# Performance work log

Measured on AMD Instinct MI355X. Metric: run time of the kernel, lower is better.

## Reference

```python
import jax, jax.numpy as jnp
import numpy as np

B, S, D, H = 4, 2048, 1024, 16
HD = D // H
EPS = 1e-5

def _ln(x, g, b):
    mu = jnp.mean(x, axis=-1, keepdims=True)
    var = jnp.mean(jnp.square(x - mu), axis=-1, keepdims=True)
    return (x - mu) * jax.lax.rsqrt(var + EPS) * g + b

def setup_inputs() -> dict:
    key = jax.random.key(0)
    ks = jax.random.split(key, 6)
    W = 0.02  # GPT-2 style init scale keeps softmax unsaturated
    causal = jnp.tril(jnp.ones((S, S), dtype=bool))
    mask = jnp.where(causal, 0.0, -1e9).astype(jnp.float32)[None, None]
    return {
        "x": jax.random.normal(ks[0], (B, S, D), jnp.float32),
        "attention_mask": mask,
        "ln1_g": jnp.ones((D,), jnp.float32),
        "ln1_b": jnp.zeros((D,), jnp.float32),
        "w_qkv": jax.random.normal(ks[1], (D, 3 * D), jnp.float32) * W,
        "b_qkv": jnp.zeros((3 * D,), jnp.float32),
        "w_ao": jax.random.normal(ks[2], (D, D), jnp.float32) * W,
        "b_ao": jnp.zeros((D,), jnp.float32),
        "ln2_g": jnp.ones((D,), jnp.float32),
        "ln2_b": jnp.zeros((D,), jnp.float32),
        "w_fc": jax.random.normal(ks[3], (D, 4 * D), jnp.float32) * W,
        "b_fc": jnp.zeros((4 * D,), jnp.float32),
        "w_out": jax.random.normal(ks[4], (4 * D, D), jnp.float32) * W,
        "b_out": jnp.zeros((D,), jnp.float32),
    }

def reference(x, attention_mask, ln1_g, ln1_b, w_qkv, b_qkv, w_ao, b_ao,
              ln2_g, ln2_b, w_fc, b_fc, w_out, b_out):
    b, s, d = x.shape
    h = _ln(x, ln1_g, ln1_b)
    qkv = h @ w_qkv + b_qkv  # [B,S,3D]
    q, k, v = jnp.split(qkv, 3, axis=-1)
    def heads(t):  # [B,S,D] -> [B,H,S,HD]
        return t.reshape(b, s, H, HD).transpose(0, 2, 1, 3)
    q, k, v = heads(q), heads(k), heads(v)
    att = jnp.einsum('bhqd,bhkd->bhqk', q, k) / jnp.sqrt(jnp.float32(HD))
    att = att + attention_mask
    att = jax.nn.softmax(att, axis=-1)
    out = jnp.einsum('bhqk,bhkd->bhqd', att, v)
    out = out.transpose(0, 2, 1, 3).reshape(b, s, d)
    x = x + out @ w_ao + b_ao
    h2 = _ln(x, ln2_g, ln2_b)
    # torch nn.GELU() default is exact erf gelu
    mlp = jax.nn.gelu(h2 @ w_fc + b_fc, approximate=False) @ w_out + b_out
    return x + mlp
```

## Files before the change

kernel.cpp:

```cpp
#include <hip/hip_runtime.h>

typedef unsigned short u16;
typedef __attribute__((ext_vector_type(8))) short short8;
typedef __attribute__((ext_vector_type(4))) float floatx4;
typedef __attribute__((ext_vector_type(4))) unsigned short ushort4_t;

#define S_LEN 2048
#define DMODEL 1024
#define NHEAD 16
#define HDIM 64

__device__ __forceinline__ u16 f2bf(float f) {
    union { float f; unsigned u; } v; v.f = f;
    unsigned u = v.u;
    unsigned r = (u + 0x7fffu + ((u >> 16) & 1u)) >> 16;
    return (u16)r;
}

__device__ __forceinline__ u16 f2bf_fast(float f) {
    union { float f; unsigned u; } v; v.f = f;
    return (u16)((v.u + 0x8000u) >> 16);
}

__device__ __forceinline__ void gld_lds16(const u16* g, u16* l) {
    __builtin_amdgcn_global_load_lds((const __attribute__((address_space(1))) void*)g,
                                     (__attribute__((address_space(3))) void*)l,
                                     16, 0, 0);
}

__global__ __launch_bounds__(256) void ln_kernel(
    const float* __restrict__ x, const float* __restrict__ g,
    const float* __restrict__ b, u16* __restrict__ out)
{
    int row = blockIdx.x;
    int tid = threadIdx.x;
    const float4* xr = (const float4*)(x + (size_t)row * DMODEL);
    float4 v = xr[tid];
    float s  = v.x + v.y + v.z + v.w;
    float s2 = v.x * v.x + v.y * v.y + v.z * v.z + v.w * v.w;
    #pragma unroll
    for (int off = 1; off < 64; off <<= 1) {
        s  += __shfl_xor(s, off, 64);
        s2 += __shfl_xor(s2, off, 64);
    }
    __shared__ float red[2][4];
    int w = tid >> 6, lane = tid & 63;
    if (lane == 0) { red[0][w] = s; red[1][w] = s2; }
    __syncthreads();
    s  = red[0][0] + red[0][1] + red[0][2] + red[0][3];
    s2 = red[1][0] + red[1][1] + red[1][2] + red[1][3];
    float mu  = s * (1.0f / DMODEL);
    float var = s2 * (1.0f / DMODEL) - mu * mu;
    float inv = rsqrtf(var + 1e-5f);
    const float4* gr = (const float4*)g;
    const float4* br = (const float4*)b;
    float4 gv = gr[tid], bv = br[tid];
    u16* o = out + (size_t)row * DMODEL + tid * 4;
    o[0] = f2bf((v.x - mu) * inv * gv.x + bv.x);
    o[1] = f2bf((v.y - mu) * inv * gv.y + bv.y);
    o[2] = f2bf((v.z - mu) * inv * gv.z + bv.z);
    o[3] = f2bf((v.w - mu) * inv * gv.w + bv.w);
}

__global__ __launch_bounds__(256) void transpose_cast(
    const float* __restrict__ w, u16* __restrict__ wt, int K, int N)
{
    __shared__ float t[32][33];
    int n0 = blockIdx.x * 32, k0 = blockIdx.y * 32;
    int x = threadIdx.x, y = threadIdx.y;
    #pragma unroll
    for (int j = y; j < 32; j += 8)
        t[j][x] = w[(size_t)(k0 + j) * N + n0 + x];
    __syncthreads();
    #pragma unroll
    for (int j = y; j < 32; j += 8)
        wt[(size_t)(n0 + j) * K + k0 + x] = f2bf(t[x][j]);
}

template<int MODE>
__global__ __launch_bounds__(256) void gemm_bt(
    const u16* __restrict__ A, const u16* __restrict__ BT,
    int M, int N, int K,
    const float* __restrict__ bias, const float* __restrict__ res,
    float* __restrict__ fout,
    u16* __restrict__ o0, u16* __restrict__ o1, u16* __restrict__ o2)
{
    __shared__ __attribute__((aligned(16))) u16 As[2][128 * 64];
    __shared__ __attribute__((aligned(16))) u16 Bs[2][128 * 64];
    int tid = threadIdx.x;
    int lane = tid & 63, w = tid >> 6;
    int wm = (w >> 1) * 64, wn = (w & 1) * 64;
    int l15 = lane & 15, quad = lane >> 4;
    int rowBase = blockIdx.y * 128, colBase = blockIdx.x * 128;

    floatx4 acc[4][4] = {};

    const u16* pa[4];
    const u16* pbt[4];
    int scb[4];
    #pragma unroll
    for (int i = 0; i < 4; ++i) {
        int c  = i * 256 + tid;
        int r  = c >> 3;
        int cs = ((c & 7) ^ (r & 7)) * 8;
        pa[i]  = A  + (size_t)(rowBase + r) * K + cs;
        pbt[i] = BT + (size_t)(colBase + r) * K + cs;
        scb[i] = (i * 256 + (tid & 0xC0)) * 8;
    }

    int KT = K >> 6;

    #pragma unroll
    for (int i = 0; i < 4; ++i) {
        gld_lds16(pa[i],  &As[0][0] + scb[i]);
        gld_lds16(pbt[i], &Bs[0][0] + scb[i]);
    }

    for (int kt = 0; kt < KT; ++kt) {
        __syncthreads();

        if (kt + 1 < KT) {
            u16* abuf = &As[(kt + 1) & 1][0];
            u16* bbuf = &Bs[(kt + 1) & 1][0];
            #pragma unroll
            for (int i = 0; i < 4; ++i) {
                pa[i]  += 64;
                pbt[i] += 64;
                gld_lds16(pa[i],  abuf + scb[i]);
                gld_lds16(pbt[i], bbuf + scb[i]);
            }
        }

        const u16* as = &As[kt & 1][0];
        const u16* bs = &Bs[kt & 1][0];
        #pragma unroll
        for (int ks = 0; ks < 2; ++ks) {
            int sw = (((ks * 4 + quad) ^ (l15 & 7))) * 8;
            short8 af[4], bf[4];
            #pragma unroll
            for (int im = 0; im < 4; ++im)
                af[im] = *(const short8*)(as + (wm + im * 16 + l15) * 64 + sw);
            #pragma unroll
            for (int in = 0; in < 4; ++in)
                bf[in] = *(const short8*)(bs + (wn + in * 16 + l15) * 64 + sw);
            #pragma unroll
            for (int im = 0; im < 4; ++im)
                #pragma unroll
                for (int in = 0; in < 4; ++in)
                    acc[im][in] = __builtin_amdgcn_mfma_f32_16x16x32_bf16(af[im], bf[in], acc[im][in], 0, 0, 0);
        }
    }

    if (MODE == 0) {
        int t = colBase >> 10;
        int cb1023 = colBase & 1023;
        if (t == 2) {
            #pragma unroll
            for (int im = 0; im < 4; ++im) {
                int gr0 = rowBase + wm + im * 16 + quad * 4;
                int bb2 = gr0 >> 11, ss = gr0 & 2047;
                #pragma unroll
                for (int in = 0; in < 4; ++in) {
                    int gc = colBase + wn + in * 16 + l15;
                    int rr = cb1023 + wn + in * 16 + l15;
                    int hh = rr >> 6, hd = rr & 63;
                    float bv = bias[gc];
                    ushort4_t pk;
                    pk.x = f2bf_fast(acc[im][in][0] + bv);
                    pk.y = f2bf_fast(acc[im][in][1] + bv);
                    pk.z = f2bf_fast(acc[im][in][2] + bv);
                    pk.w = f2bf_fast(acc[im][in][3] + bv);
                    *(ushort4_t*)(o1 + ((size_t)(bb2 * NHEAD + hh) * HDIM + hd) * S_LEN + ss) = pk;
                }
            }
        } else {
            u16* qb = o0 + (size_t)t * 8388608;
            float sc = (t == 0) ? 0.125f : 1.0f;
            #pragma unroll
            for (int im = 0; im < 4; ++im) {
                #pragma unroll
                for (int in = 0; in < 4; ++in) {
                    #pragma unroll
                    for (int r = 0; r < 4; ++r) {
                        int gr = rowBase + wm + im * 16 + quad * 4 + r;
                        int gc = colBase + wn + in * 16 + l15;
                        float v = (acc[im][in][r] + bias[gc]) * sc;
                        int rr = cb1023 + wn + in * 16 + l15;
                        int hh = rr >> 6, hd = rr & 63;
                        int bb2 = gr >> 11, ss = gr & 2047;
                        qb[(((size_t)(bb2 * NHEAD + hh) * S_LEN + ss) * HDIM) + hd] = f2bf_fast(v);
                    }
                }
            }
        }
    } else {
        #pragma unroll
        for (int im = 0; im < 4; ++im) {
            #pragma unroll
            for (int in = 0; in < 4; ++in) {
                #pragma unroll
                for (int r = 0; r < 4; ++r) {
                    int gr = rowBase + wm + im * 16 + quad * 4 + r;
                    int gc = colBase + wn + in * 16 + l15;
                    float v = acc[im][in][r] + bias[gc];
                    if (MODE == 2) {
                        float p = v * (1.59576912f + 0.07135481f * v * v);
                        float e = __expf(-p);
                        float gl = v * __builtin_amdgcn_rcpf(1.0f + e);
                        o0[(size_t)gr * N + gc] = f2bf_fast(gl);
                    } else {
                        fout[(size_t)gr * N + gc] = v + res[(size_t)gr * N + gc];
                    }
                }
            }
        }
    }
}

__global__ __launch_bounds__(256) void flash_attn(
    const u16* __restrict__ Q, const u16* __restrict__ Kb,
    const u16* __restrict__ Vt, u16* __restrict__ O)
{
    __shared__ __attribute__((aligned(16))) u16 Ks[2][64 * 64];
    __shared__ __attribute__((aligned(16))) u16 Vs[2][64 * 64];
    __shared__ __attribute__((aligned(16))) u16 Pl[4][2][16][64];
    int tid = threadIdx.x;
    int lane = tid & 63, w = tid >> 6;
    int l15 = lane & 15, quad = lane >> 4;
    int bh = blockIdx.x;
    int pp = blockIdx.y;
    int bb = bh >> 4, h = bh & 15;

    const u16* Kp0 = Kb + (size_t)bh * S_LEN * HDIM;
    const u16* Vp  = Vt + (size_t)bh * HDIM * S_LEN;

    int rstage = lane >> 3;
    int cstage = ((lane & 7) ^ rstage) * 8;
    int vrow0  = w * 8 + rstage;

    int ms[2] = {pp, 15 - pp};
    int pb = 0;

    #pragma unroll
    for (int i = 0; i < 2; ++i) {
        int row = i * 32 + vrow0;
        gld_lds16(Kp0 + row * HDIM + cstage, &Ks[0][0] + i * 2048 + w * 512);
        gld_lds16(Vp + (size_t)row * S_LEN + cstage, &Vs[0][0] + i * 2048 + w * 512);
    }

    #pragma unroll 1
    for (int sel = 0; sel < 2; ++sel) {
        int m = ms[sel];
        int q0 = m * 128;

        const u16* Qp = Q + ((size_t)bh * S_LEN + q0 + w * 16) * HDIM;
        short8 aq0[2], aq1[2];
        #pragma unroll
        for (int ks = 0; ks < 2; ++ks) {
            aq0[ks] = *(const short8*)(Qp + l15 * HDIM + ks * 32 + quad * 8);
            aq1[ks] = *(const short8*)(Qp + 64 * HDIM + l15 * HDIM + ks * 32 + quad * 8);
        }

        floatx4 acc_o0[4] = {}, acc_o1[4] = {};
        float rs0[4] = {0.f, 0.f, 0.f, 0.f};
        float rs1[4] = {0.f, 0.f, 0.f, 0.f};

        int KT = 2 * m + 2;

        auto softmax_store = [&](floatx4 (&sa)[4], float (&rs)[4], int st, bool diag) {
            #pragma unroll
            for (int nt = 0; nt < 4; ++nt) {
                int wc = nt * 16 + l15;
                int wchunk = wc >> 3, woff = wc & 7;
                #pragma unroll
                for (int r = 0; r < 4; ++r) {
                    float sv = sa[nt][r];
                    if (diag) {
                        int qr = w * 16 + quad * 4 + r;
                        if (wc > qr) sv = -1e30f;
                    }
                    float pv = __expf(sv);
                    rs[r] += pv;
                    int row = quad * 4 + r;
                    Pl[w][st][row][((wchunk ^ (row & 7)) << 3) + woff] = f2bf_fast(pv);
                }
            }
        };

        #pragma unroll 1
        for (int kt = 0; kt < KT; ++kt) {
            __syncthreads();
            int cur = pb;

            int nk = (kt + 1 < KT) ? (kt + 1) : ((sel < 1) ? 0 : -1);
            if (nk >= 0) {
                pb ^= 1;
                const u16* Kg = Kp0 + (size_t)nk * 64 * HDIM;
                const u16* Vg = Vp + nk * 64;
                u16* kb_ = &Ks[pb][0];
                u16* vb_ = &Vs[pb][0];
                #pragma unroll
                for (int i = 0; i < 2; ++i) {
                    int row = i * 32 + vrow0;
                    gld_lds16(Kg + row * HDIM + cstage, kb_ + i * 2048 + w * 512);
                    gld_lds16(Vg + (size_t)row * S_LEN + cstage, vb_ + i * 2048 + w * 512);
                }
            }

            const u16* kcur = &Ks[cur][0];
            const u16* vcur = &Vs[cur][0];

            bool a0 = (kt < KT - 1);

            floatx4 s0a[4] = {}, s1a[4] = {};
            __builtin_amdgcn_s_setprio(1);
            #pragma unroll
            for (int nt = 0; nt < 4; ++nt) {
                #pragma unroll
                for (int ks = 0; ks < 2; ++ks) {
                    int sw = ((ks * 4 + quad) ^ (l15 & 7)) * 8;
                    short8 bk = *(const short8*)(kcur + (nt * 16 + l15) * 64 + sw);
                    s0a[nt] = __builtin_amdgcn_mfma_f32_16x16x32_bf16(aq0[ks], bk, s0a[nt], 0, 0, 0);
                    s1a[nt] = __builtin_amdgcn_mfma_f32_16x16x32_bf16(aq1[ks], bk, s1a[nt], 0, 0, 0);
                }
            }
            __builtin_amdgcn_s_setprio(0);

            if (a0) softmax_store(s0a, rs0, 0, kt == KT - 2);
            softmax_store(s1a, rs1, 1, kt == KT - 1);

            short8 pf0[2] = {}, pf1[2];
            if (a0) {
                #pragma unroll
                for (int ks = 0; ks < 2; ++ks) {
                    int pc = ((ks * 4 + quad) ^ (l15 & 7)) * 8;
                    pf0[ks] = *(const short8*)(&Pl[w][0][l15][pc]);
                }
            }
            #pragma unroll
            for (int ks = 0; ks < 2; ++ks) {
                int pc = ((ks * 4 + quad) ^ (l15 & 7)) * 8;
                pf1[ks] = *(const short8*)(&Pl[w][1][l15][pc]);
            }

            __builtin_amdgcn_s_setprio(1);
            #pragma unroll
            for (int nt = 0; nt < 4; ++nt) {
                #pragma unroll
                for (int ks = 0; ks < 2; ++ks) {
                    int sw = ((ks * 4 + quad) ^ (l15 & 7)) * 8;
                    short8 bv = *(const short8*)(vcur + (nt * 16 + l15) * 64 + sw);
                    acc_o0[nt] = __builtin_amdgcn_mfma_f32_16x16x32_bf16(pf0[ks], bv, acc_o0[nt], 0, 0, 0);
                    acc_o1[nt] = __builtin_amdgcn_mfma_f32_16x16x32_bf16(pf1[ks], bv, acc_o1[nt], 0, 0, 0);
                }
            }
            __builtin_amdgcn_s_setprio(0);
        }

        float inv0[4], inv1[4];
        #pragma unroll
        for (int r = 0; r < 4; ++r) {
            float sm0 = rs0[r], sm1 = rs1[r];
            #pragma unroll
            for (int off = 1; off < 16; off <<= 1) {
                sm0 += __shfl_xor(sm0, off, 64);
                sm1 += __shfl_xor(sm1, off, 64);
            }
            inv0[r] = 1.0f / sm0;
            inv1[r] = 1.0f / sm1;
        }

        #pragma unroll
        for (int nt = 0; nt < 4; ++nt) {
            #pragma unroll
            for (int r = 0; r < 4; ++r) {
                int qr = q0 + w * 16 + quad * 4 + r;
                int hd = nt * 16 + l15;
                O[((size_t)bb * S_LEN + qr) * DMODEL + h * HDIM + hd] = f2bf(acc_o0[nt][r] * inv0[r]);
                O[((size_t)bb * S_LEN + qr + 64) * DMODEL + h * HDIM + hd] = f2bf(acc_o1[nt][r] * inv1[r]);
            }
        }
    }
}

extern "C" void kernel_launch(void* const* d_in, const int* in_sizes, int n_in,
                              void* d_out, int out_size, void* d_ws, size_t ws_size,
                              hipStream_t stream)
{
    const float* x    = (const float*)d_in[0];
    const float* ln1g = (const float*)d_in[2];
    const float* ln1b = (const float*)d_in[3];
    const float* wqkv = (const float*)d_in[4];
    const float* bqkv = (const float*)d_in[5];
    const float* wao  = (const float*)d_in[6];
    const float* bao  = (const float*)d_in[7];
    const float* ln2g = (const float*)d_in[8];
    const float* ln2b = (const float*)d_in[9];
    const float* wfc  = (const float*)d_in[10];
    const float* bfc  = (const float*)d_in[11];
    const float* wout = (const float*)d_in[12];
    const float* bout = (const float*)d_in[13];
    float* out = (float*)d_out;

    char* ws = (char*)d_ws;
    u16* wqkvT = (u16*)(ws + 0);
    u16* waoT  = (u16*)(ws + 6291456);
    u16* wfcT  = (u16*)(ws + 8388608);
    u16* woutT = (u16*)(ws + 16777216);
    u16* hb    = (u16*)(ws + 25165824);
    u16* QKVb  = (u16*)(ws + 41943040);
    u16* Vtb   = (u16*)(ws + 92274688);
    u16* Gb    = (u16*)(ws + 41943040);

    u16* Qb   = QKVb;
    u16* Kbuf = QKVb + 8388608;

    transpose_cast<<<dim3(3072/32, 1024/32), dim3(32, 8), 0, stream>>>(wqkv, wqkvT, 1024, 3072);
    transpose_cast<<<dim3(1024/32, 1024/32), dim3(32, 8), 0, stream>>>(wao,  waoT,  1024, 1024);
    transpose_cast<<<dim3(4096/32, 1024/32), dim3(32, 8), 0, stream>>>(wfc,  wfcT,  1024, 4096);
    transpose_cast<<<dim3(1024/32, 4096/32), dim3(32, 8), 0, stream>>>(wout, woutT, 4096, 1024);

    ln_kernel<<<8192, 256, 0, stream>>>(x, ln1g, ln1b, hb);

    gemm_bt<0><<<dim3(3072/128, 8192/128), 256, 0, stream>>>(
        hb, wqkvT, 8192, 3072, 1024, bqkv, nullptr, nullptr, QKVb, Vtb, nullptr);

    flash_attn<<<dim3(64, 8), 256, 0, stream>>>(Qb, Kbuf, Vtb, hb);

    gemm_bt<1><<<dim3(1024/128, 8192/128), 256, 0, stream>>>(
        hb, waoT, 8192, 1024, 1024, bao, x, out, nullptr, nullptr, nullptr);

    ln_kernel<<<8192, 256, 0, stream>>>(out, ln2g, ln2b, hb);

    gemm_bt<2><<<dim3(4096/128, 8192/128), 256, 0, stream>>>(
        hb, wfcT, 8192, 4096, 1024, bfc, nullptr, nullptr, Gb, nullptr, nullptr);

    gemm_bt<3><<<dim3(1024/128, 8192/128), 256, 0, stream>>>(
        Gb, woutT, 8192, 1024, 4096, bout, out, out, nullptr, nullptr, nullptr);
}
```

Baseline: 498.0 us.

## Add 256x256 8-wave ping-pong GEMM for QKV and FC projections

Adds a new 512-thread GEMM kernel with 256x256 output tiles, double-buffered LDS split into halves, and an eight-phase schedule that interleaves global-to-LDS prefetch with MFMA quadrants, using barriers and s_setprio. The QKV and FC1+GELU GEMMs now use it, while the older 128x128 kernel is reduced to the residual-add epilogue for the remaining GEMMs. The larger tiles are meant to raise arithmetic intensity and overlap memory with compute. In exchange, register pressure and LDS use are higher, and fewer blocks are launched for the QKV shape.

Result: slower. 511.0 us (+2.6%).

```diff
diff --git a/kernel.cpp b/kernel.cpp
--- a/kernel.cpp
+++ b/kernel.cpp
@@ -151,25 +151,152 @@
         }
     }
 
+    #pragma unroll
+    for (int im = 0; im < 4; ++im) {
+        #pragma unroll
+        for (int in = 0; in < 4; ++in) {
+            #pragma unroll
+            for (int r = 0; r < 4; ++r) {
+                int gr = rowBase + wm + im * 16 + quad * 4 + r;
+                int gc = colBase + wn + in * 16 + l15;
+                float v = acc[im][in][r] + bias[gc];
+                fout[(size_t)gr * N + gc] = v + res[(size_t)gr * N + gc];
+            }
+        }
+    }
+}
+
+template<int MODE>
+__global__ __launch_bounds__(512, 2) void gemm256(
+    const u16* __restrict__ A, const u16* __restrict__ BT,
+    int M, int N, int K,
+    const float* __restrict__ bias,
+    u16* __restrict__ o0, u16* __restrict__ o1)
+{
+    __shared__ __attribute__((aligned(16))) u16 As[2][2][128 * 64];
+    __shared__ __attribute__((aligned(16))) u16 Bs[2][2][128 * 64];
+    int tid = threadIdx.x;
+    int lane = tid & 63, w = tid >> 6;
+    int wrow = w >> 2, wcol = w & 3;
+    int l15 = lane & 15, quad = lane >> 4;
+    int rowBase = blockIdx.y * 256, colBase = blockIdx.x * 256;
+    int nrb = (wcol & 1) * 64;
+
+    int swz[2] = { (quad ^ (l15 & 7)) * 8, ((4 + quad) ^ (l15 & 7)) * 8 };
+
+    int cid0 = tid, cid1 = 512 + tid;
+    int r0 = cid0 >> 3, r1 = cid1 >> 3;
+    unsigned cs0 = (unsigned)(((cid0 & 7) ^ (r0 & 7)) * 8);
+    unsigned cs1 = (unsigned)(((cid1 & 7) ^ (r1 & 7)) * 8);
+    unsigned aoff0 = (unsigned)((rowBase + r0) * K) + cs0;
+    unsigned aoff1 = (unsigned)((rowBase + r1) * K) + cs1;
+    unsigned boff0 = (unsigned)((colBase + r0) * K) + cs0;
+    unsigned boff1 = (unsigned)((colBase + r1) * K) + cs1;
+    unsigned ldo0 = (unsigned)(cid0 * 8), ldo1 = (unsigned)(cid1 * 8);
+    unsigned hK = (unsigned)(128 * K);
+
+    floatx4 acc[8][4] = {};
+    short8 af[4][2], bfL[2][2], bfH[2][2];
+
+    int KT = K >> 6;
+
+#define STG_A(db, tt, h) do { unsigned tb_ = (unsigned)(tt) * 64u + (h) * hK;      \
+    gld_lds16(A + aoff0 + tb_, &As[db][h][0] + ldo0);                              \
+    gld_lds16(A + aoff1 + tb_, &As[db][h][0] + ldo1); } while (0)
+#define STG_B(db, tt, h) do { unsigned tb_ = (unsigned)(tt) * 64u + (h) * hK;      \
+    gld_lds16(BT + boff0 + tb_, &Bs[db][h][0] + ldo0);                             \
+    gld_lds16(BT + boff1 + tb_, &Bs[db][h][0] + ldo1); } while (0)
+#define LDS_A(buf, MFB) do { const u16* ap_ = &As[buf][wrow][0];                   \
+    _Pragma("unroll") for (int m_ = 0; m_ < 4; ++m_) {                             \
+      af[m_][0] = *(const short8*)(ap_ + (((MFB) + m_) * 16 + l15) * 64 + swz[0]); \
+      af[m_][1] = *(const short8*)(ap_ + (((MFB) + m_) * 16 + l15) * 64 + swz[1]); } } while (0)
+#define LDS_B(buf, NFP, dst) do { const u16* bp_ = &Bs[buf][wcol >> 1][0];         \
+    _Pragma("unroll") for (int n_ = 0; n_ < 2; ++n_) {                             \
+      dst[n_][0] = *(const short8*)(bp_ + (nrb + ((NFP) * 2 + n_) * 16 + l15) * 64 + swz[0]); \
+      dst[n_][1] = *(const short8*)(bp_ + (nrb + ((NFP) * 2 + n_) * 16 + l15) * 64 + swz[1]); } } while (0)
+#define MFMA_Q(MFB, NFP, bsrc) do { __builtin_amdgcn_s_setprio(1);                 \
+    _Pragma("unroll") for (int m_ = 0; m_ < 4; ++m_)                               \
+    _Pragma("unroll") for (int n_ = 0; n_ < 2; ++n_) {                             \
+      acc[(MFB) + m_][(NFP) * 2 + n_] = __builtin_amdgcn_mfma_f32_16x16x32_bf16(af[m_][0], bsrc[n_][0], acc[(MFB) + m_][(NFP) * 2 + n_], 0, 0, 0); \
+      acc[(MFB) + m_][(NFP) * 2 + n_] = __builtin_amdgcn_mfma_f32_16x16x32_bf16(af[m_][1], bsrc[n_][1], acc[(MFB) + m_][(NFP) * 2 + n_], 0, 0, 0); } \
+    __builtin_amdgcn_s_setprio(0); } while (0)
+#define PH_MID() do { __builtin_amdgcn_s_barrier();                                \
+    asm volatile("s_waitcnt lgkmcnt(0)" ::: "memory"); } while (0)
+#define PH_END() __builtin_amdgcn_s_barrier()
+
+    STG_A(0, 0, 0); STG_A(0, 0, 1);
+    STG_B(0, 0, 0); STG_B(0, 0, 1);
+    STG_B(1, 1, 0); STG_B(1, 1, 1);
+    asm volatile("s_waitcnt vmcnt(4)" ::: "memory");
+    __builtin_amdgcn_s_barrier();
+
+    for (int t = 0; t < KT; t += 2) {
+        int t2 = (t + 2 < KT) ? t + 2 : KT - 1;
+        int t3 = (t + 3 < KT) ? t + 3 : KT - 1;
+
+        LDS_A(0, 0); LDS_B(0, 0, bfL);
+        STG_A(1, t + 1, 0);
+        PH_MID(); MFMA_Q(0, 0, bfL); PH_END();
+
+        LDS_B(0, 1, bfH);
+        STG_A(1, t + 1, 1);
+        PH_MID(); MFMA_Q(0, 1, bfH); PH_END();
+
+        LDS_A(0, 4);
+        STG_B(0, t2, 0);
+        PH_MID(); MFMA_Q(4, 1, bfH); PH_END();
+
+        STG_B(0, t2, 1);
+        asm volatile("s_waitcnt vmcnt(4)" ::: "memory");
+        PH_MID(); MFMA_Q(4, 0, bfL); PH_END();
+
+        LDS_A(1, 0); LDS_B(1, 0, bfL);
+        STG_A(0, t2, 0);
+        PH_MID(); MFMA_Q(0, 0, bfL); PH_END();
+
+        LDS_B(1, 1, bfH);
+        STG_A(0, t2, 1);
+        PH_MID(); MFMA_Q(0, 1, bfH); PH_END();
+
+        LDS_A(1, 4);
+        STG_B(1, t3, 0);
+        PH_MID(); MFMA_Q(4, 1, bfH); PH_END();
+
+        STG_B(1, t3, 1);
+        asm volatile("s_waitcnt vmcnt(4)" ::: "memory");
+        PH_MID(); MFMA_Q(4, 0, bfL); PH_END();
+    }
+    asm volatile("s_waitcnt vmcnt(0)" ::: "memory");
+
+#undef STG_A
+#undef STG_B
+#undef LDS_A
+#undef LDS_B
+#undef MFMA_Q
+#undef PH_MID
+#undef PH_END
+
+    int wr0 = rowBase + wrow * 128 + quad * 4;
+    int wc0 = colBase + wcol * 64 + l15;
     if (MODE == 0) {
         int t = colBase >> 10;
-        int cb1023 = colBase & 1023;
+        int cb1023 = (colBase & 1023) + wcol * 64;
         if (t == 2) {
             #pragma unroll
-            for (int im = 0; im < 4; ++im) {
-                int gr0 = rowBase + wm + im * 16 + quad * 4;
+            for (int mf = 0; mf < 8; ++mf) {
+                int gr0 = wr0 + mf * 16;
                 int bb2 = gr0 >> 11, ss = gr0 & 2047;
                 #pragma unroll
-                for (int in = 0; in < 4; ++in) {
-                    int gc = colBase + wn + in * 16 + l15;
-                    int rr = cb1023 + wn + in * 16 + l15;
+                for (int nf = 0; nf < 4; ++nf) {
+                    int gc = wc0 + nf * 16;
+                    int rr = cb1023 + nf * 16 + l15;
                     int hh = rr >> 6, hd = rr & 63;
                     float bv = bias[gc];
                     ushort4_t pk;
-                    pk.x = f2bf_fast(acc[im][in][0] + bv);
-                    pk.y = f2bf_fast(acc[im][in][1] + bv);
-                    pk.z = f2bf_fast(acc[im][in][2] + bv);
-                    pk.w = f2bf_fast(acc[im][in][3] + bv);
+                    pk.x = f2bf_fast(acc[mf][nf][0] + bv);
+                    pk.y = f2bf_fast(acc[mf][nf][1] + bv);
+                    pk.z = f2bf_fast(acc[mf][nf][2] + bv);
+                    pk.w = f2bf_fast(acc[mf][nf][3] + bv);
                     *(ushort4_t*)(o1 + ((size_t)(bb2 * NHEAD + hh) * HDIM + hd) * S_LEN + ss) = pk;
                 }
             }
@@ -177,16 +304,16 @@
             u16* qb = o0 + (size_t)t * 8388608;
             float sc = (t == 0) ? 0.125f : 1.0f;
             #pragma unroll
-            for (int im = 0; im < 4; ++im) {
-                #pragma unroll
-                for (int in = 0; in < 4; ++in) {
+            for (int mf = 0; mf < 8; ++mf) {
+                #pragma unroll
+                for (int nf = 0; nf < 4; ++nf) {
+                    int gc = wc0 + nf * 16;
+                    int rr = cb1023 + nf * 16 + l15;
+                    int hh = rr >> 6, hd = rr & 63;
                     #pragma unroll
                     for (int r = 0; r < 4; ++r) {
-                        int gr = rowBase + wm + im * 16 + quad * 4 + r;
-                        int gc = colBase + wn + in * 16 + l15;
-                        float v = (acc[im][in][r] + bias[gc]) * sc;
-                        int rr = cb1023 + wn + in * 16 + l15;
-                        int hh = rr >> 6, hd = rr & 63;
+                        int gr = wr0 + mf * 16 + r;
+                        float v = (acc[mf][nf][r] + bias[gc]) * sc;
                         int bb2 = gr >> 11, ss = gr & 2047;
                         qb[(((size_t)(bb2 * NHEAD + hh) * S_LEN + ss) * HDIM) + hd] = f2bf_fast(v);
                     }
@@ -195,22 +322,19 @@
         }
     } else {
         #pragma unroll
-        for (int im = 0; im < 4; ++im) {
-            #pragma unroll
-            for (int in = 0; in < 4; ++in) {
+        for (int mf = 0; mf < 8; ++mf) {
+            #pragma unroll
+            for (int nf = 0; nf < 4; ++nf) {
+                int gc = wc0 + nf * 16;
+                float bv = bias[gc];
                 #pragma unroll
                 for (int r = 0; r < 4; ++r) {
-                    int gr = rowBase + wm + im * 16 + quad * 4 + r;
-                    int gc = colBase + wn + in * 16 + l15;
-                    float v = acc[im][in][r] + bias[gc];
-                    if (MODE == 2) {
-                        float p = v * (1.59576912f + 0.07135481f * v * v);
-                        float e = __expf(-p);
-                        float gl = v * __builtin_amdgcn_rcpf(1.0f + e);
-                        o0[(size_t)gr * N + gc] = f2bf_fast(gl);
-                    } else {
-                        fout[(size_t)gr * N + gc] = v + res[(size_t)gr * N + gc];
-                    }
+                    int gr = wr0 + mf * 16 + r;
+                    float v = acc[mf][nf][r] + bv;
+                    float p = v * (1.59576912f + 0.07135481f * v * v);
+                    float e = __expf(-p);
+                    float gl = v * __builtin_amdgcn_rcpf(1.0f + e);
+                    o0[(size_t)gr * N + gc] = f2bf_fast(gl);
                 }
             }
         }
@@ -422,8 +546,8 @@
 
     ln_kernel<<<8192, 256, 0, stream>>>(x, ln1g, ln1b, hb);
 
-    gemm_bt<0><<<dim3(3072/128, 8192/128), 256, 0, stream>>>(
-        hb, wqkvT, 8192, 3072, 1024, bqkv, nullptr, nullptr, QKVb, Vtb, nullptr);
+    gemm256<0><<<dim3(3072/256, 8192/256), 512, 0, stream>>>(
+        hb, wqkvT, 8192, 3072, 1024, bqkv, QKVb, Vtb);
 
     flash_attn<<<dim3(64, 8), 256, 0, stream>>>(Qb, Kbuf, Vtb, hb);
 
@@ -432,8 +556,8 @@
 
     ln_kernel<<<8192, 256, 0, stream>>>(out, ln2g, ln2b, hb);
 
-    gemm_bt<2><<<dim3(4096/128, 8192/128), 256, 0, stream>>>(
-        hb, wfcT, 8192, 4096, 1024, bfc, nullptr, nullptr, Gb, nullptr, nullptr);
+    gemm256<2><<<dim3(4096/256, 8192/256), 512, 0, stream>>>(
+        hb, wfcT, 8192, 4096, 1024, bfc, Gb, nullptr);
 
     gemm_bt<3><<<dim3(1024/128, 8192/128), 256, 0, stream>>>(
         Gb, woutT, 8192, 1024, 4096, bout, out, out, nullptr, nullptr, nullptr);
```
